# Performance work log

Measured on AMD Instinct MI355X. Metric: run time of the kernel, lower is better.

## Reference

```python
import jax, jax.numpy as jnp
import numpy as np


def make_dictionary(T, Drr, Dtheta):
    # rows i=0..T-1; (-Drr)**i == (-1)**i * Drr**i for integer i
    idx = jnp.arange(T, dtype=Drr.dtype)[:, None]                      # [T,1]
    sign = jnp.where(jnp.arange(T)[:, None] % 2 == 0, 1.0, -1.0).astype(Drr.dtype)
    ri = Drr[None, :] ** idx                                           # [T,N]
    c = jnp.cos(idx * Dtheta[None, :])
    s = jnp.sin(idx * Dtheta[None, :])
    dic = jnp.concatenate(
        [jnp.ones((T, 1), Drr.dtype), ri * c, sign * ri * c, ri * s, sign * ri * s],
        axis=1,
    )                                                                  # [T, 1+4N]
    G = jnp.linalg.norm(dic, axis=0)
    G = jnp.where(G == 0, jnp.sqrt(jnp.asarray(T, dic.dtype)), G)
    return dic / G


def softshrink(x, lam):
    return jnp.sign(x) * jnp.maximum(jnp.abs(x) - lam, 0.0)


def fista(D, Y, lambd=0.1, max_iter=100, tol=1e-4):
    # D: [T,K], Y: [B,T,F]
    K = D.shape[1]
    DtD = D.T @ D                                                      # [K,K]
    linv = 1.0 / jnp.linalg.norm(DtD)  # torch.norm(DtD, 2) == Frobenius norm
    DtY = jnp.einsum('tk,btf->bkf', D, Y) * linv                       # [B,K,F]
    A = jnp.eye(K, dtype=D.dtype) - DtD * linv
    lam = lambd * linv
    x0 = jnp.zeros_like(DtY)

    def cond(s):
        _, _, _, it, done = s
        return (it < max_iter) & jnp.logical_not(done)

    def body(s):
        x_old, y_old, t, it, done = s
        x_new = softshrink(jnp.einsum('kj,bjf->bkf', A, y_old) + DtY, lam)
        t_new = (1.0 + jnp.sqrt(1.0 + 4.0 * t * t)) / 2.0
        tt = (t - 1.0) / t_new
        y_new = (1.0 + tt) * x_new - tt * x_old
        conv = jnp.linalg.norm((x_new - x_old).ravel()) / K < tol
        return (x_new, y_new, jnp.where(conv, t, t_new), it + 1, conv)

    s0 = (x0, x0, jnp.asarray(1.0, D.dtype), jnp.asarray(0, jnp.int32),
          jnp.asarray(False))
    x, _, _, _, _ = jax.lax.while_loop(cond, body, s0)
    return x


def setup_inputs() -> dict:
    key = jax.random.key(0)
    k1, k2, k3 = jax.random.split(key, 3)
    return {
        'x': jax.random.normal(k1, (2, 36, 20480), jnp.float32),
        'Drr': jax.random.uniform(k2, (40,), dtype=jnp.float32),
        'Dtheta': jax.random.uniform(k3, (40,), dtype=jnp.float32),
        'T': 36,
    }


def reference(x, Drr, Dtheta, T):
    D = make_dictionary(T, Drr, Dtheta)
    return fista(D, x, lambd=0.1, max_iter=100)
```

## Files before the change

kernel.cpp:

```cpp
#include <hip/hip_runtime.h>
#include <math.h>

typedef _Float16 half8 __attribute__((ext_vector_type(8)));
typedef _Float16 half4 __attribute__((ext_vector_type(4)));
typedef __fp16   fp16x2 __attribute__((ext_vector_type(2)));
typedef float    f32x4 __attribute__((ext_vector_type(4)));

#define T_DIM 36
#define N_AT 40
#define K_REAL 161
#define MT 11
#define KSM 5
#define KS2 2
#define B_DIM 2
#define F_DIM 20480
#define CB 32
#define NTHREADS 256
#define SETUP_T 512
#define MAXIT 100
#define YK 200
#define YST 72

#define WS_AFRAG_OFF 64
#define AFRAG_BYTES (MT * KSM * 2 * 1024)
#define WS_DFRAG_OFF (WS_AFRAG_OFF + AFRAG_BYTES)
#define DFRAG_BYTES (MT * KS2 * 2 * 1024)
#define WS_A160_OFF (WS_DFRAG_OFF + DFRAG_BYTES)

#define MFMA16(a, b, c) __builtin_amdgcn_mfma_f32_16x16x32_f16((a), (b), (c), 0, 0, 0)

__global__ void setup_kernel(const float* __restrict__ Drr,
                             const float* __restrict__ Dtheta,
                             float* __restrict__ ws) {
    __shared__ float Dl[K_REAL][T_DIM];
    __shared__ float red[SETUP_T];
    __shared__ float s_linv;
    int tid = threadIdx.x;

    if (tid < K_REAL) {
        float col[T_DIM];
        if (tid == 0) {
            for (int i = 0; i < T_DIM; ++i) col[i] = 1.0f;
        } else {
            int q = (tid - 1) / N_AT, n = (tid - 1) % N_AT;
            float r = Drr[n], th = Dtheta[n];
            float ri = 1.0f;
            for (int i = 0; i < T_DIM; ++i) {
                float c = cosf((float)i * th), s = sinf((float)i * th);
                float sign = (i & 1) ? -1.0f : 1.0f;
                float v;
                if (q == 0)      v = ri * c;
                else if (q == 1) v = sign * ri * c;
                else if (q == 2) v = ri * s;
                else             v = sign * ri * s;
                col[i] = v;
                ri *= r;
            }
        }
        float ss = 0.0f;
        for (int i = 0; i < T_DIM; ++i) ss += col[i] * col[i];
        float G = sqrtf(ss);
        float Ginv = (G == 0.0f) ? (1.0f / sqrtf((float)T_DIM)) : (1.0f / G);
        for (int i = 0; i < T_DIM; ++i) Dl[tid][i] = col[i] * Ginv;
    }
    __syncthreads();

    float local = 0.0f;
    for (int p = tid; p < K_REAL * K_REAL; p += SETUP_T) {
        int a = p / K_REAL, b = p % K_REAL;
        float dot = 0.0f;
        for (int i = 0; i < T_DIM; ++i) dot += Dl[a][i] * Dl[b][i];
        local += dot * dot;
    }
    red[tid] = local;
    __syncthreads();
    if (tid == 0) {
        float tot = 0.0f;
        for (int i = 0; i < SETUP_T; ++i) tot += red[i];
        float linv = 1.0f / sqrtf(tot);
        s_linv = linv;
        ws[0] = linv;
        ws[1] = 0.1f * linv;
    }
    __syncthreads();
    float linv = s_linv;

    _Float16* wsA = (_Float16*)((char*)ws + WS_AFRAG_OFF);
    int lane = tid >> 3, e = tid & 7;
    int fm = lane & 15, fq = lane >> 4;
    for (int p = 0; p < MT * KSM; ++p) {
        int Mt = p / KSM, ks = p % KSM;
        int m = Mt * 16 + fm;
        int k = ks * 32 + fq * 8 + e;
        float v = 0.0f;
        if (m < K_REAL) {
            float dot = 0.0f;
            for (int t = 0; t < T_DIM; ++t) dot += Dl[m][t] * Dl[k][t];
            v = ((m == k) ? 1.0f : 0.0f) - linv * dot;
        }
        _Float16 h = (_Float16)v;
        _Float16 l = (_Float16)(v - (float)h);
        int base = (p * 2) * 512 + lane * 8 + e;
        wsA[base]       = h;
        wsA[base + 512] = l;
    }

    _Float16* wsD = (_Float16*)((char*)ws + WS_DFRAG_OFF);
    for (int p = 0; p < MT * KS2; ++p) {
        int Mt = p / KS2, ks2 = p % KS2;
        int kr = Mt * 16 + fm;
        int t  = ks2 * 32 + fq * 8 + e;
        float v = (kr < K_REAL && t < T_DIM) ? linv * Dl[kr][t] : 0.0f;
        _Float16 h = (_Float16)v;
        _Float16 l = (_Float16)(v - (float)h);
        int base = (p * 2) * 512 + lane * 8 + e;
        wsD[base]       = h;
        wsD[base + 512] = l;
    }

    float* wsC = (float*)((char*)ws + WS_A160_OFF);
    if (tid < MT * 16) {
        int m = tid;
        float v = 0.0f;
        if (m < K_REAL) {
            float dot = 0.0f;
            for (int t = 0; t < T_DIM; ++t) dot += Dl[m][t] * Dl[160][t];
            v = ((m == 160) ? 1.0f : 0.0f) - linv * dot;
        }
        wsC[m] = v;
    }
}

template <int G>
__device__ __forceinline__ void sweep_g(f32x4 (&acc)[3], const f32x4 (&dty)[3],
                                        const half8 (&Af)[3][KSM][2],
                                        const float (&a160)[3][4],
                                        const _Float16 (*Yh)[YK],
                                        const _Float16 (*Yl)[YK],
                                        int cl, int quad, int mlc) {
    #pragma unroll
    for (int ks = 0; ks < KSM; ++ks) {
        half8 yh = *(const half8*)&Yh[G * 16 + cl][ks * 32 + quad * 8];
        half8 yl = *(const half8*)&Yl[G * 16 + cl][ks * 32 + quad * 8];
        #pragma unroll
        for (int ml = 0; ml < 3; ++ml) {
            if (ml < mlc) {
                f32x4 c0 = (ks == 0) ? dty[ml] : acc[ml];
                c0 = MFMA16(Af[ml][ks][0], yh, c0);
                c0 = MFMA16(Af[ml][ks][0], yl, c0);
                acc[ml] = MFMA16(Af[ml][ks][1], yh, c0);
            }
        }
    }
    float y160 = (float)Yh[G * 16 + cl][160] + (float)Yl[G * 16 + cl][160];
    #pragma unroll
    for (int ml = 0; ml < 3; ++ml)
        if (ml < mlc)
            #pragma unroll
            for (int r = 0; r < 4; ++r)
                acc[ml][r] += a160[ml][r] * y160;
}

template <int G>
__device__ __forceinline__ void epi_g(const f32x4 (&acc)[3], float (&xold)[3][4],
                                      _Float16 (*Yh)[YK], _Float16 (*Yl)[YK],
                                      float lam, float tt,
                                      int cl, int quad, int mg, int mlc) {
    #pragma unroll
    for (int ml = 0; ml < 3; ++ml) {
        if (ml < mlc) {
            float yn[4];
            #pragma unroll
            for (int r = 0; r < 4; ++r) {
                float v  = acc[ml][r];
                float s  = fmaxf(fabsf(v) - lam, 0.0f);
                float xn = copysignf(s, v);
                yn[r] = xn + tt * (xn - xold[ml][r]);
                xold[ml][r] = xn;
            }
            fp16x2 h01 = __builtin_amdgcn_cvt_pkrtz(yn[0], yn[1]);
            fp16x2 h23 = __builtin_amdgcn_cvt_pkrtz(yn[2], yn[3]);
            float l0 = yn[0] - (float)h01[0];
            float l1 = yn[1] - (float)h01[1];
            float l2 = yn[2] - (float)h23[0];
            float l3 = yn[3] - (float)h23[1];
            fp16x2 l01 = __builtin_amdgcn_cvt_pkrtz(l0, l1);
            fp16x2 l23 = __builtin_amdgcn_cvt_pkrtz(l2, l3);
            half4 hv, lv;
            hv[0] = (_Float16)h01[0]; hv[1] = (_Float16)h01[1];
            hv[2] = (_Float16)h23[0]; hv[3] = (_Float16)h23[1];
            lv[0] = (_Float16)l01[0]; lv[1] = (_Float16)l01[1];
            lv[2] = (_Float16)l23[0]; lv[3] = (_Float16)l23[1];
            int k0 = (mg * 3 + ml) * 16 + quad * 4;
            *(half4*)&Yh[G * 16 + cl][k0] = hv;
            *(half4*)&Yl[G * 16 + cl][k0] = lv;
        }
    }
}

__global__ void __launch_bounds__(NTHREADS, 2)
fista_mfma(const float* __restrict__ Y, const float* __restrict__ ws,
           float* __restrict__ out) {
    __shared__ __align__(16) _Float16 Yh[CB][YK];
    __shared__ __align__(16) _Float16 Yl[CB][YK];

    const float lam = ((const float*)ws)[1];
    const half8* Afp = (const half8*)((const char*)ws + WS_AFRAG_OFF);
    const half8* Dfp = (const half8*)((const char*)ws + WS_DFRAG_OFF);
    const float* A160 = (const float*)((const char*)ws + WS_A160_OFF);

    const int tid  = threadIdx.x;
    const int lane = tid & 63;
    const int mg   = __builtin_amdgcn_readfirstlane(tid >> 6);
    const int mlc  = (mg == 3) ? 2 : 3;
    const int quad = lane >> 4;
    const int cl   = lane & 15;

    const int blk = blockIdx.x;
    const int b   = blk / (F_DIM / CB);
    const int f0  = (blk % (F_DIM / CB)) * CB;

    _Float16* sh = &Yh[0][0];
    _Float16* sl = &Yl[0][0];
    const float* Yb = Y + (size_t)b * T_DIM * F_DIM + f0;
    for (int idx = tid; idx < 64 * CB; idx += NTHREADS) {
        int t = idx / CB, c = idx % CB;
        float v = (t < T_DIM) ? Yb[(size_t)t * F_DIM + c] : 0.0f;
        _Float16 h = (_Float16)v;
        _Float16 l = (_Float16)(v - (float)h);
        sh[c * YST + t] = h;
        sl[c * YST + t] = l;
    }
    __syncthreads();

    f32x4 dty[2][3];
    #pragma unroll
    for (int g = 0; g < 2; ++g)
        #pragma unroll
        for (int ml = 0; ml < 3; ++ml) dty[g][ml] = f32x4{0.f, 0.f, 0.f, 0.f};
    #pragma unroll
    for (int ks2 = 0; ks2 < KS2; ++ks2) {
        #pragma unroll
        for (int g = 0; g < 2; ++g) {
            half8 yh = *(const half8*)&sh[(g * 16 + cl) * YST + ks2 * 32 + quad * 8];
            half8 yl = *(const half8*)&sl[(g * 16 + cl) * YST + ks2 * 32 + quad * 8];
            #pragma unroll
            for (int ml = 0; ml < 3; ++ml) {
                if (ml < mlc) {
                    int Mt = mg * 3 + ml;
                    half8 dh = Dfp[((Mt * KS2 + ks2) * 2 + 0) * 64 + lane];
                    half8 dl = Dfp[((Mt * KS2 + ks2) * 2 + 1) * 64 + lane];
                    dty[g][ml] = MFMA16(dh, yh, dty[g][ml]);
                    dty[g][ml] = MFMA16(dh, yl, dty[g][ml]);
                    dty[g][ml] = MFMA16(dl, yh, dty[g][ml]);
                }
            }
        }
    }
    __syncthreads();

    {
        int4* z1 = (int4*)&Yh[0][0];
        int4* z2 = (int4*)&Yl[0][0];
        for (int idx = tid; idx < (CB * YK * 2) / 16; idx += NTHREADS) {
            z1[idx] = int4{0, 0, 0, 0};
            z2[idx] = int4{0, 0, 0, 0};
        }
    }

    half8 Af[3][KSM][2];
    float a160[3][4];
    #pragma unroll
    for (int ml = 0; ml < 3; ++ml) {
        if (ml < mlc) {
            #pragma unroll
            for (int ks = 0; ks < KSM; ++ks)
                #pragma unroll
                for (int term = 0; term < 2; ++term)
                    Af[ml][ks][term] =
                        Afp[(((mg * 3 + ml) * KSM + ks) * 2 + term) * 64 + lane];
            #pragma unroll
            for (int r = 0; r < 4; ++r)
                a160[ml][r] = A160[(mg * 3 + ml) * 16 + quad * 4 + r];
        }
    }
    __syncthreads();

    float xoldA[3][4], xoldB[3][4];
    #pragma unroll
    for (int ml = 0; ml < 3; ++ml)
        #pragma unroll
        for (int r = 0; r < 4; ++r) { xoldA[ml][r] = 0.0f; xoldB[ml][r] = 0.0f; }

    f32x4 accA[3], accB[3];
    #pragma unroll
    for (int ml = 0; ml < 3; ++ml) { accA[ml] = dty[0][ml]; accB[ml] = dty[1][ml]; }

    float tm = 1.61803398875f;
    float tt_prev = 0.0f;

    epi_g<0>(accA, xoldA, Yh, Yl, lam, tt_prev, cl, quad, mg, mlc);
    __syncthreads();

    for (int s = 2; s <= MAXIT; ++s) {
        float tn = 0.5f * (1.0f + sqrtf(1.0f + 4.0f * tm * tm));
        float tt_cur = (tm - 1.0f) / tn;
        tm = tn;

        sweep_g<0>(accA, dty[0], Af, a160, Yh, Yl, cl, quad, mlc);
        epi_g<1>(accB, xoldB, Yh, Yl, lam, tt_prev, cl, quad, mg, mlc);
        __syncthreads();

        sweep_g<1>(accB, dty[1], Af, a160, Yh, Yl, cl, quad, mlc);
        epi_g<0>(accA, xoldA, Yh, Yl, lam, tt_cur, cl, quad, mg, mlc);
        __syncthreads();

        tt_prev = tt_cur;
    }
    epi_g<1>(accB, xoldB, Yh, Yl, lam, tt_prev, cl, quad, mg, mlc);

    #pragma unroll
    for (int g = 0; g < 2; ++g) {
        float* ob = out + (size_t)b * K_REAL * F_DIM + f0 + g * 16 + cl;
        #pragma unroll
        for (int ml = 0; ml < 3; ++ml)
            if (ml < mlc)
                #pragma unroll
                for (int r = 0; r < 4; ++r) {
                    int k = (mg * 3 + ml) * 16 + quad * 4 + r;
                    float xv = g ? xoldB[ml][r] : xoldA[ml][r];
                    if (k < K_REAL) ob[(size_t)k * F_DIM] = xv;
                }
    }
}

extern "C" void kernel_launch(void* const* d_in, const int* in_sizes, int n_in,
                              void* d_out, int out_size, void* d_ws, size_t ws_size,
                              hipStream_t stream) {
    const float* x      = (const float*)d_in[0];
    const float* Drr    = (const float*)d_in[1];
    const float* Dtheta = (const float*)d_in[2];
    float* out = (float*)d_out;
    float* ws  = (float*)d_ws;

    hipLaunchKernelGGL(setup_kernel, dim3(1), dim3(SETUP_T), 0, stream,
                       Drr, Dtheta, ws);
    hipLaunchKernelGGL(fista_mfma, dim3((B_DIM * F_DIM) / CB), dim3(NTHREADS),
                       0, stream, x, ws, out);
}
```

Measured before the change: 674.2 us.

## Switch FISTA iteration to 32x32 MFMA with double-buffered swizzled LDS

Replaces the 16x16x32 MFMA tiling (4 waves, two interleaved column groups, separate k=160 scalar fixup) with 32x32x16 MFMA tiles across 6 waves covering K padded to 192. The Y iterate is double-buffered in LDS with an XOR swizzle, so each iteration needs one barrier instead of two. The goal is fewer MFMA issues per FLOP, no scalar tail correction, fewer bank conflicts and less synchronisation. The cost is padding waste (192 vs 161 rows), more threads per block and higher register pressure from the 16-wide accumulators and 22 A fragments, plus a change in occupancy target.

```diff
diff --git a/kernel.cpp b/kernel.cpp
--- a/kernel.cpp
+++ b/kernel.cpp
@@ -4,30 +4,29 @@
 typedef _Float16 half8 __attribute__((ext_vector_type(8)));
 typedef _Float16 half4 __attribute__((ext_vector_type(4)));
 typedef __fp16   fp16x2 __attribute__((ext_vector_type(2)));
-typedef float    f32x4 __attribute__((ext_vector_type(4)));
+typedef float    f32x16 __attribute__((ext_vector_type(16)));
 
 #define T_DIM 36
 #define N_AT 40
 #define K_REAL 161
-#define MT 11
-#define KSM 5
-#define KS2 2
+#define MT2 6
+#define KS 11
+#define TKS 3
 #define B_DIM 2
 #define F_DIM 20480
 #define CB 32
-#define NTHREADS 256
+#define NTHREADS 384
 #define SETUP_T 512
 #define MAXIT 100
 #define YK 200
 #define YST 72
 
 #define WS_AFRAG_OFF 64
-#define AFRAG_BYTES (MT * KSM * 2 * 1024)
+#define AFRAG_BYTES (MT2 * KS * 2 * 1024)
 #define WS_DFRAG_OFF (WS_AFRAG_OFF + AFRAG_BYTES)
-#define DFRAG_BYTES (MT * KS2 * 2 * 1024)
-#define WS_A160_OFF (WS_DFRAG_OFF + DFRAG_BYTES)
-
-#define MFMA16(a, b, c) __builtin_amdgcn_mfma_f32_16x16x32_f16((a), (b), (c), 0, 0, 0)
+#define DFRAG_BYTES (MT2 * TKS * 2 * 1024)
+
+#define MFMA32(a, b, c) __builtin_amdgcn_mfma_f32_32x32x16_f16((a), (b), (c), 0, 0, 0)
 
 __global__ void setup_kernel(const float* __restrict__ Drr,
                              const float* __restrict__ Dtheta,
@@ -87,13 +86,13 @@
 
     _Float16* wsA = (_Float16*)((char*)ws + WS_AFRAG_OFF);
     int lane = tid >> 3, e = tid & 7;
-    int fm = lane & 15, fq = lane >> 4;
-    for (int p = 0; p < MT * KSM; ++p) {
-        int Mt = p / KSM, ks = p % KSM;
-        int m = Mt * 16 + fm;
-        int k = ks * 32 + fq * 8 + e;
+    int lm = lane & 31, lhi = lane >> 5;
+    for (int p = 0; p < MT2 * KS; ++p) {
+        int Mt = p / KS, ks = p % KS;
+        int m = Mt * 32 + lm;
+        int k = ks * 16 + lhi * 8 + e;
         float v = 0.0f;
-        if (m < K_REAL) {
+        if (m < K_REAL && k < K_REAL) {
             float dot = 0.0f;
             for (int t = 0; t < T_DIM; ++t) dot += Dl[m][t] * Dl[k][t];
             v = ((m == k) ? 1.0f : 0.0f) - linv * dot;
@@ -106,10 +105,10 @@
     }
 
     _Float16* wsD = (_Float16*)((char*)ws + WS_DFRAG_OFF);
-    for (int p = 0; p < MT * KS2; ++p) {
-        int Mt = p / KS2, ks2 = p % KS2;
-        int kr = Mt * 16 + fm;
-        int t  = ks2 * 32 + fq * 8 + e;
+    for (int p = 0; p < MT2 * TKS; ++p) {
+        int Mt = p / TKS, ks2 = p % TKS;
+        int kr = Mt * 32 + lm;
+        int t  = ks2 * 16 + lhi * 8 + e;
         float v = (kr < K_REAL && t < T_DIM) ? linv * Dl[kr][t] : 0.0f;
         _Float16 h = (_Float16)v;
         _Float16 l = (_Float16)(v - (float)h);
@@ -117,221 +116,143 @@
         wsD[base]       = h;
         wsD[base + 512] = l;
     }
-
-    float* wsC = (float*)((char*)ws + WS_A160_OFF);
-    if (tid < MT * 16) {
-        int m = tid;
-        float v = 0.0f;
-        if (m < K_REAL) {
-            float dot = 0.0f;
-            for (int t = 0; t < T_DIM; ++t) dot += Dl[m][t] * Dl[160][t];
-            v = ((m == 160) ? 1.0f : 0.0f) - linv * dot;
-        }
-        wsC[m] = v;
-    }
-}
-
-template <int G>
-__device__ __forceinline__ void sweep_g(f32x4 (&acc)[3], const f32x4 (&dty)[3],
-                                        const half8 (&Af)[3][KSM][2],
-                                        const float (&a160)[3][4],
-                                        const _Float16 (*Yh)[YK],
-                                        const _Float16 (*Yl)[YK],
-                                        int cl, int quad, int mlc) {
-    #pragma unroll
-    for (int ks = 0; ks < KSM; ++ks) {
-        half8 yh = *(const half8*)&Yh[G * 16 + cl][ks * 32 + quad * 8];
-        half8 yl = *(const half8*)&Yl[G * 16 + cl][ks * 32 + quad * 8];
-        #pragma unroll
-        for (int ml = 0; ml < 3; ++ml) {
-            if (ml < mlc) {
-                f32x4 c0 = (ks == 0) ? dty[ml] : acc[ml];
-                c0 = MFMA16(Af[ml][ks][0], yh, c0);
-                c0 = MFMA16(Af[ml][ks][0], yl, c0);
-                acc[ml] = MFMA16(Af[ml][ks][1], yh, c0);
-            }
-        }
-    }
-    float y160 = (float)Yh[G * 16 + cl][160] + (float)Yl[G * 16 + cl][160];
-    #pragma unroll
-    for (int ml = 0; ml < 3; ++ml)
-        if (ml < mlc)
-            #pragma unroll
-            for (int r = 0; r < 4; ++r)
-                acc[ml][r] += a160[ml][r] * y160;
-}
-
-template <int G>
-__device__ __forceinline__ void epi_g(const f32x4 (&acc)[3], float (&xold)[3][4],
-                                      _Float16 (*Yh)[YK], _Float16 (*Yl)[YK],
-                                      float lam, float tt,
-                                      int cl, int quad, int mg, int mlc) {
-    #pragma unroll
-    for (int ml = 0; ml < 3; ++ml) {
-        if (ml < mlc) {
-            float yn[4];
-            #pragma unroll
-            for (int r = 0; r < 4; ++r) {
-                float v  = acc[ml][r];
-                float s  = fmaxf(fabsf(v) - lam, 0.0f);
-                float xn = copysignf(s, v);
-                yn[r] = xn + tt * (xn - xold[ml][r]);
-                xold[ml][r] = xn;
-            }
-            fp16x2 h01 = __builtin_amdgcn_cvt_pkrtz(yn[0], yn[1]);
-            fp16x2 h23 = __builtin_amdgcn_cvt_pkrtz(yn[2], yn[3]);
-            float l0 = yn[0] - (float)h01[0];
-            float l1 = yn[1] - (float)h01[1];
-            float l2 = yn[2] - (float)h23[0];
-            float l3 = yn[3] - (float)h23[1];
-            fp16x2 l01 = __builtin_amdgcn_cvt_pkrtz(l0, l1);
-            fp16x2 l23 = __builtin_amdgcn_cvt_pkrtz(l2, l3);
-            half4 hv, lv;
-            hv[0] = (_Float16)h01[0]; hv[1] = (_Float16)h01[1];
-            hv[2] = (_Float16)h23[0]; hv[3] = (_Float16)h23[1];
-            lv[0] = (_Float16)l01[0]; lv[1] = (_Float16)l01[1];
-            lv[2] = (_Float16)l23[0]; lv[3] = (_Float16)l23[1];
-            int k0 = (mg * 3 + ml) * 16 + quad * 4;
-            *(half4*)&Yh[G * 16 + cl][k0] = hv;
-            *(half4*)&Yl[G * 16 + cl][k0] = lv;
-        }
-    }
-}
-
-__global__ void __launch_bounds__(NTHREADS, 2)
+}
+
+__device__ __forceinline__ void epi_write(const f32x16& acc, float (&xold)[16],
+                                          _Float16* rowH, _Float16* rowL,
+                                          float lam, float tt,
+                                          int wv, int sw, int hi) {
+    #pragma unroll
+    for (int g = 0; g < 4; ++g) {
+        float yn[4];
+        #pragma unroll
+        for (int i = 0; i < 4; ++i) {
+            int r = g * 4 + i;
+            float v  = acc[r];
+            float s  = fmaxf(fabsf(v) - lam, 0.0f);
+            float xn = copysignf(s, v);
+            yn[i] = xn + tt * (xn - xold[r]);
+            xold[r] = xn;
+        }
+        fp16x2 h01 = __builtin_amdgcn_cvt_pkrtz(yn[0], yn[1]);
+        fp16x2 h23 = __builtin_amdgcn_cvt_pkrtz(yn[2], yn[3]);
+        float l0 = yn[0] - (float)h01[0];
+        float l1 = yn[1] - (float)h01[1];
+        float l2 = yn[2] - (float)h23[0];
+        float l3 = yn[3] - (float)h23[1];
+        fp16x2 l01 = __builtin_amdgcn_cvt_pkrtz(l0, l1);
+        fp16x2 l23 = __builtin_amdgcn_cvt_pkrtz(l2, l3);
+        half4 hv, lv;
+        hv[0] = (_Float16)h01[0]; hv[1] = (_Float16)h01[1];
+        hv[2] = (_Float16)h23[0]; hv[3] = (_Float16)h23[1];
+        lv[0] = (_Float16)l01[0]; lv[1] = (_Float16)l01[1];
+        lv[2] = (_Float16)l23[0]; lv[3] = (_Float16)l23[1];
+        int boff = (((wv * 4 + g) ^ sw) << 4) + (hi << 3);
+        *(half4*)((char*)rowH + boff) = hv;
+        *(half4*)((char*)rowL + boff) = lv;
+    }
+}
+
+__global__ void __launch_bounds__(NTHREADS, 3)
 fista_mfma(const float* __restrict__ Y, const float* __restrict__ ws,
            float* __restrict__ out) {
-    __shared__ __align__(16) _Float16 Yh[CB][YK];
-    __shared__ __align__(16) _Float16 Yl[CB][YK];
+    __shared__ __align__(16) _Float16 Yb_lds[2][2][CB][YK];
 
     const float lam = ((const float*)ws)[1];
     const half8* Afp = (const half8*)((const char*)ws + WS_AFRAG_OFF);
     const half8* Dfp = (const half8*)((const char*)ws + WS_DFRAG_OFF);
-    const float* A160 = (const float*)((const char*)ws + WS_A160_OFF);
 
     const int tid  = threadIdx.x;
     const int lane = tid & 63;
-    const int mg   = __builtin_amdgcn_readfirstlane(tid >> 6);
-    const int mlc  = (mg == 3) ? 2 : 3;
-    const int quad = lane >> 4;
-    const int cl   = lane & 15;
+    const int wv   = __builtin_amdgcn_readfirstlane(tid >> 6);
+    const int c    = lane & 31;
+    const int hi   = lane >> 5;
+    const int sw   = (c >> 3) & 3;
 
     const int blk = blockIdx.x;
     const int b   = blk / (F_DIM / CB);
     const int f0  = (blk % (F_DIM / CB)) * CB;
 
-    _Float16* sh = &Yh[0][0];
-    _Float16* sl = &Yl[0][0];
+    _Float16* sh = &Yb_lds[0][0][0][0];
+    _Float16* sl = &Yb_lds[0][1][0][0];
     const float* Yb = Y + (size_t)b * T_DIM * F_DIM + f0;
-    for (int idx = tid; idx < 64 * CB; idx += NTHREADS) {
-        int t = idx / CB, c = idx % CB;
-        float v = (t < T_DIM) ? Yb[(size_t)t * F_DIM + c] : 0.0f;
+    for (int idx = tid; idx < 48 * CB; idx += NTHREADS) {
+        int t = idx >> 5, cc = idx & 31;
+        float v = (t < T_DIM) ? Yb[(size_t)t * F_DIM + cc] : 0.0f;
         _Float16 h = (_Float16)v;
         _Float16 l = (_Float16)(v - (float)h);
-        sh[c * YST + t] = h;
-        sl[c * YST + t] = l;
-    }
-    __syncthreads();
-
-    f32x4 dty[2][3];
-    #pragma unroll
-    for (int g = 0; g < 2; ++g)
-        #pragma unroll
-        for (int ml = 0; ml < 3; ++ml) dty[g][ml] = f32x4{0.f, 0.f, 0.f, 0.f};
-    #pragma unroll
-    for (int ks2 = 0; ks2 < KS2; ++ks2) {
-        #pragma unroll
-        for (int g = 0; g < 2; ++g) {
-            half8 yh = *(const half8*)&sh[(g * 16 + cl) * YST + ks2 * 32 + quad * 8];
-            half8 yl = *(const half8*)&sl[(g * 16 + cl) * YST + ks2 * 32 + quad * 8];
-            #pragma unroll
-            for (int ml = 0; ml < 3; ++ml) {
-                if (ml < mlc) {
-                    int Mt = mg * 3 + ml;
-                    half8 dh = Dfp[((Mt * KS2 + ks2) * 2 + 0) * 64 + lane];
-                    half8 dl = Dfp[((Mt * KS2 + ks2) * 2 + 1) * 64 + lane];
-                    dty[g][ml] = MFMA16(dh, yh, dty[g][ml]);
-                    dty[g][ml] = MFMA16(dh, yl, dty[g][ml]);
-                    dty[g][ml] = MFMA16(dl, yh, dty[g][ml]);
-                }
-            }
-        }
-    }
-    __syncthreads();
-
-    {
-        int4* z1 = (int4*)&Yh[0][0];
-        int4* z2 = (int4*)&Yl[0][0];
-        for (int idx = tid; idx < (CB * YK * 2) / 16; idx += NTHREADS) {
-            z1[idx] = int4{0, 0, 0, 0};
-            z2[idx] = int4{0, 0, 0, 0};
-        }
-    }
-
-    half8 Af[3][KSM][2];
-    float a160[3][4];
-    #pragma unroll
-    for (int ml = 0; ml < 3; ++ml) {
-        if (ml < mlc) {
-            #pragma unroll
-            for (int ks = 0; ks < KSM; ++ks)
-                #pragma unroll
-                for (int term = 0; term < 2; ++term)
-                    Af[ml][ks][term] =
-                        Afp[(((mg * 3 + ml) * KSM + ks) * 2 + term) * 64 + lane];
-            #pragma unroll
-            for (int r = 0; r < 4; ++r)
-                a160[ml][r] = A160[(mg * 3 + ml) * 16 + quad * 4 + r];
-        }
-    }
-    __syncthreads();
-
-    float xoldA[3][4], xoldB[3][4];
-    #pragma unroll
-    for (int ml = 0; ml < 3; ++ml)
-        #pragma unroll
-        for (int r = 0; r < 4; ++r) { xoldA[ml][r] = 0.0f; xoldB[ml][r] = 0.0f; }
-
-    f32x4 accA[3], accB[3];
-    #pragma unroll
-    for (int ml = 0; ml < 3; ++ml) { accA[ml] = dty[0][ml]; accB[ml] = dty[1][ml]; }
+        sh[cc * YST + t] = h;
+        sl[cc * YST + t] = l;
+    }
+    __syncthreads();
+
+    f32x16 dty;
+    #pragma unroll
+    for (int i = 0; i < 16; ++i) dty[i] = 0.0f;
+    #pragma unroll
+    for (int ks2 = 0; ks2 < TKS; ++ks2) {
+        half8 yh = *(const half8*)&sh[c * YST + ks2 * 16 + hi * 8];
+        half8 yl = *(const half8*)&sl[c * YST + ks2 * 16 + hi * 8];
+        half8 dh = Dfp[((wv * TKS + ks2) * 2 + 0) * 64 + lane];
+        half8 dl = Dfp[((wv * TKS + ks2) * 2 + 1) * 64 + lane];
+        dty = MFMA32(dh, yh, dty);
+        dty = MFMA32(dh, yl, dty);
+        dty = MFMA32(dl, yh, dty);
+    }
+    __syncthreads();
+
+    half8 Af[KS][2];
+    #pragma unroll
+    for (int ks = 0; ks < KS; ++ks)
+        #pragma unroll
+        for (int term = 0; term < 2; ++term)
+            Af[ks][term] = Afp[((wv * KS + ks) * 2 + term) * 64 + lane];
+
+    float xold[16];
+    #pragma unroll
+    for (int r = 0; r < 16; ++r) xold[r] = 0.0f;
+
+    f32x16 acc = dty;
 
     float tm = 1.61803398875f;
-    float tt_prev = 0.0f;
-
-    epi_g<0>(accA, xoldA, Yh, Yl, lam, tt_prev, cl, quad, mg, mlc);
+
+    epi_write(acc, xold, &Yb_lds[0][0][c][0], &Yb_lds[0][1][c][0],
+              lam, 0.0f, wv, sw, hi);
     __syncthreads();
 
     for (int s = 2; s <= MAXIT; ++s) {
         float tn = 0.5f * (1.0f + sqrtf(1.0f + 4.0f * tm * tm));
-        float tt_cur = (tm - 1.0f) / tn;
+        float tt = (tm - 1.0f) / tn;
         tm = tn;
 
-        sweep_g<0>(accA, dty[0], Af, a160, Yh, Yl, cl, quad, mlc);
-        epi_g<1>(accB, xoldB, Yh, Yl, lam, tt_prev, cl, quad, mg, mlc);
+        const int p = s & 1;
+        const _Float16* rH = &Yb_lds[p][0][c][0];
+        const _Float16* rL = &Yb_lds[p][1][c][0];
+
+        #pragma unroll
+        for (int ks = 0; ks < KS; ++ks) {
+            int boff = ((2 * ks + hi) ^ sw) << 4;
+            half8 yh = *(const half8*)((const char*)rH + boff);
+            half8 yl = *(const half8*)((const char*)rL + boff);
+            f32x16 c0 = (ks == 0) ? dty : acc;
+            c0  = MFMA32(Af[ks][0], yh, c0);
+            c0  = MFMA32(Af[ks][0], yl, c0);
+            acc = MFMA32(Af[ks][1], yh, c0);
+        }
+
+        epi_write(acc, xold, &Yb_lds[p ^ 1][0][c][0], &Yb_lds[p ^ 1][1][c][0],
+                  lam, tt, wv, sw, hi);
         __syncthreads();
-
-        sweep_g<1>(accB, dty[1], Af, a160, Yh, Yl, cl, quad, mlc);
-        epi_g<0>(accA, xoldA, Yh, Yl, lam, tt_cur, cl, quad, mg, mlc);
-        __syncthreads();
-
-        tt_prev = tt_cur;
-    }
-    epi_g<1>(accB, xoldB, Yh, Yl, lam, tt_prev, cl, quad, mg, mlc);
-
-    #pragma unroll
-    for (int g = 0; g < 2; ++g) {
-        float* ob = out + (size_t)b * K_REAL * F_DIM + f0 + g * 16 + cl;
-        #pragma unroll
-        for (int ml = 0; ml < 3; ++ml)
-            if (ml < mlc)
-                #pragma unroll
-                for (int r = 0; r < 4; ++r) {
-                    int k = (mg * 3 + ml) * 16 + quad * 4 + r;
-                    float xv = g ? xoldB[ml][r] : xoldA[ml][r];
-                    if (k < K_REAL) ob[(size_t)k * F_DIM] = xv;
-                }
-    }
+    }
+
+    float* ob = out + (size_t)b * K_REAL * F_DIM + f0 + c;
+    #pragma unroll
+    for (int g = 0; g < 4; ++g)
+        #pragma unroll
+        for (int i = 0; i < 4; ++i) {
+            int k = wv * 32 + i + 8 * g + 4 * hi;
+            if (k < K_REAL) ob[(size_t)k * F_DIM] = xold[g * 4 + i];
+        }
 }
 
 extern "C" void kernel_launch(void* const* d_in, const int* in_sizes, int n_in,
```

Measured after the change: 915.5 us. 35.8% more time.

## Spread M-tiles over six waves and XOR-swizzle the LDS Y layout

Applied to the files above, without the earlier changes.

The block grows from 4 to 6 waves, each now owning 2 of the 11 M-tiles instead of 3, with launch bounds raised to 3 blocks per CU. This cuts per-wave MFMA work and register use per iteration and adds latency hiding. The shared Y buffers now use a 256-half row stride with an XOR swizzle on 16-byte chunks, to avoid LDS bank conflicts in both the sweep reads and the epilogue writes. The hi/lo fp16 split now uses plain casts instead of packed round-toward-zero converts. The trade-offs are more barrier participants, an uneven last wave that owns only one tile, and slightly different rounding in the split.

```diff
diff --git a/kernel.cpp b/kernel.cpp
--- a/kernel.cpp
+++ b/kernel.cpp
@@ -3,7 +3,6 @@
 
 typedef _Float16 half8 __attribute__((ext_vector_type(8)));
 typedef _Float16 half4 __attribute__((ext_vector_type(4)));
-typedef __fp16   fp16x2 __attribute__((ext_vector_type(2)));
 typedef float    f32x4 __attribute__((ext_vector_type(4)));
 
 #define T_DIM 36
@@ -15,10 +14,10 @@
 #define B_DIM 2
 #define F_DIM 20480
 #define CB 32
-#define NTHREADS 256
+#define NTHREADS 384
 #define SETUP_T 512
 #define MAXIT 100
-#define YK 200
+#define YROW 256
 #define YST 72
 
 #define WS_AFRAG_OFF 64
@@ -132,18 +131,22 @@
 }
 
 template <int G>
-__device__ __forceinline__ void sweep_g(f32x4 (&acc)[3], const f32x4 (&dty)[3],
-                                        const half8 (&Af)[3][KSM][2],
-                                        const float (&a160)[3][4],
-                                        const _Float16 (*Yh)[YK],
-                                        const _Float16 (*Yl)[YK],
+__device__ __forceinline__ void sweep_g(f32x4 (&acc)[2], const f32x4 (&dty)[2],
+                                        const half8 (&Af)[2][KSM][2],
+                                        const float (&a160)[2][4],
+                                        const _Float16* __restrict__ Yhp,
+                                        const _Float16* __restrict__ Ylp,
                                         int cl, int quad, int mlc) {
+    const int r  = G * 16 + cl;
+    const int rb = r * YROW;
+    const int sw = r & 7;
     #pragma unroll
     for (int ks = 0; ks < KSM; ++ks) {
-        half8 yh = *(const half8*)&Yh[G * 16 + cl][ks * 32 + quad * 8];
-        half8 yl = *(const half8*)&Yl[G * 16 + cl][ks * 32 + quad * 8];
-        #pragma unroll
-        for (int ml = 0; ml < 3; ++ml) {
+        int off = rb + (((ks * 4 + quad) ^ sw) << 3);
+        half8 yh = *(const half8*)&Yhp[off];
+        half8 yl = *(const half8*)&Ylp[off];
+        #pragma unroll
+        for (int ml = 0; ml < 2; ++ml) {
             if (ml < mlc) {
                 f32x4 c0 = (ks == 0) ? dty[ml] : acc[ml];
                 c0 = MFMA16(Af[ml][ks][0], yh, c0);
@@ -152,57 +155,53 @@
             }
         }
     }
-    float y160 = (float)Yh[G * 16 + cl][160] + (float)Yl[G * 16 + cl][160];
-    #pragma unroll
-    for (int ml = 0; ml < 3; ++ml)
+    int off160 = rb + ((20 ^ sw) << 3);
+    float y160 = (float)Yhp[off160] + (float)Ylp[off160];
+    #pragma unroll
+    for (int ml = 0; ml < 2; ++ml)
         if (ml < mlc)
             #pragma unroll
-            for (int r = 0; r < 4; ++r)
-                acc[ml][r] += a160[ml][r] * y160;
+            for (int rr = 0; rr < 4; ++rr)
+                acc[ml][rr] += a160[ml][rr] * y160;
 }
 
 template <int G>
-__device__ __forceinline__ void epi_g(const f32x4 (&acc)[3], float (&xold)[3][4],
-                                      _Float16 (*Yh)[YK], _Float16 (*Yl)[YK],
+__device__ __forceinline__ void epi_g(const f32x4 (&acc)[2], float (&xold)[2][4],
+                                      _Float16* __restrict__ Yhp,
+                                      _Float16* __restrict__ Ylp,
                                       float lam, float tt,
-                                      int cl, int quad, int mg, int mlc) {
-    #pragma unroll
-    for (int ml = 0; ml < 3; ++ml) {
+                                      int cl, int quad, int wv, int mlc) {
+    const int r  = G * 16 + cl;
+    const int rb = r * YROW;
+    const int sw = r & 7;
+    #pragma unroll
+    for (int ml = 0; ml < 2; ++ml) {
         if (ml < mlc) {
-            float yn[4];
-            #pragma unroll
-            for (int r = 0; r < 4; ++r) {
-                float v  = acc[ml][r];
+            half4 hv, lv;
+            #pragma unroll
+            for (int rr = 0; rr < 4; ++rr) {
+                float v  = acc[ml][rr];
                 float s  = fmaxf(fabsf(v) - lam, 0.0f);
                 float xn = copysignf(s, v);
-                yn[r] = xn + tt * (xn - xold[ml][r]);
-                xold[ml][r] = xn;
+                float yn = xn + tt * (xn - xold[ml][rr]);
+                xold[ml][rr] = xn;
+                _Float16 h = (_Float16)yn;
+                hv[rr] = h;
+                lv[rr] = (_Float16)(yn - (float)h);
             }
-            fp16x2 h01 = __builtin_amdgcn_cvt_pkrtz(yn[0], yn[1]);
-            fp16x2 h23 = __builtin_amdgcn_cvt_pkrtz(yn[2], yn[3]);
-            float l0 = yn[0] - (float)h01[0];
-            float l1 = yn[1] - (float)h01[1];
-            float l2 = yn[2] - (float)h23[0];
-            float l3 = yn[3] - (float)h23[1];
-            fp16x2 l01 = __builtin_amdgcn_cvt_pkrtz(l0, l1);
-            fp16x2 l23 = __builtin_amdgcn_cvt_pkrtz(l2, l3);
-            half4 hv, lv;
-            hv[0] = (_Float16)h01[0]; hv[1] = (_Float16)h01[1];
-            hv[2] = (_Float16)h23[0]; hv[3] = (_Float16)h23[1];
-            lv[0] = (_Float16)l01[0]; lv[1] = (_Float16)l01[1];
-            lv[2] = (_Float16)l23[0]; lv[3] = (_Float16)l23[1];
-            int k0 = (mg * 3 + ml) * 16 + quad * 4;
-            *(half4*)&Yh[G * 16 + cl][k0] = hv;
-            *(half4*)&Yl[G * 16 + cl][k0] = lv;
-        }
-    }
-}
-
-__global__ void __launch_bounds__(NTHREADS, 2)
+            int bib = (wv * 2 + ml) * 32 + quad * 8;
+            int off = rb + ((((bib >> 4) ^ sw) << 3) | ((bib & 15) >> 1));
+            *(half4*)&Yhp[off] = hv;
+            *(half4*)&Ylp[off] = lv;
+        }
+    }
+}
+
+__global__ void __launch_bounds__(NTHREADS, 3)
 fista_mfma(const float* __restrict__ Y, const float* __restrict__ ws,
            float* __restrict__ out) {
-    __shared__ __align__(16) _Float16 Yh[CB][YK];
-    __shared__ __align__(16) _Float16 Yl[CB][YK];
+    __shared__ __align__(16) _Float16 YhL[CB * YROW];
+    __shared__ __align__(16) _Float16 YlL[CB * YROW];
 
     const float lam = ((const float*)ws)[1];
     const half8* Afp = (const half8*)((const char*)ws + WS_AFRAG_OFF);
@@ -211,8 +210,8 @@
 
     const int tid  = threadIdx.x;
     const int lane = tid & 63;
-    const int mg   = __builtin_amdgcn_readfirstlane(tid >> 6);
-    const int mlc  = (mg == 3) ? 2 : 3;
+    const int wv   = __builtin_amdgcn_readfirstlane(tid >> 6);
+    const int mlc  = (wv == 5) ? 1 : 2;
     const int quad = lane >> 4;
     const int cl   = lane & 15;
 
@@ -220,8 +219,8 @@
     const int b   = blk / (F_DIM / CB);
     const int f0  = (blk % (F_DIM / CB)) * CB;
 
-    _Float16* sh = &Yh[0][0];
-    _Float16* sl = &Yl[0][0];
+    _Float16* sh = &YhL[0];
+    _Float16* sl = &YlL[0];
     const float* Yb = Y + (size_t)b * T_DIM * F_DIM + f0;
     for (int idx = tid; idx < 64 * CB; idx += NTHREADS) {
         int t = idx / CB, c = idx % CB;
@@ -233,11 +232,11 @@
     }
     __syncthreads();
 
-    f32x4 dty[2][3];
+    f32x4 dty[2][2];
     #pragma unroll
     for (int g = 0; g < 2; ++g)
         #pragma unroll
-        for (int ml = 0; ml < 3; ++ml) dty[g][ml] = f32x4{0.f, 0.f, 0.f, 0.f};
+        for (int ml = 0; ml < 2; ++ml) dty[g][ml] = f32x4{0.f, 0.f, 0.f, 0.f};
     #pragma unroll
     for (int ks2 = 0; ks2 < KS2; ++ks2) {
         #pragma unroll
@@ -245,9 +244,9 @@
             half8 yh = *(const half8*)&sh[(g * 16 + cl) * YST + ks2 * 32 + quad * 8];
             half8 yl = *(const half8*)&sl[(g * 16 + cl) * YST + ks2 * 32 + quad * 8];
             #pragma unroll
-            for (int ml = 0; ml < 3; ++ml) {
+            for (int ml = 0; ml < 2; ++ml) {
                 if (ml < mlc) {
-                    int Mt = mg * 3 + ml;
+                    int Mt = wv * 2 + ml;
                     half8 dh = Dfp[((Mt * KS2 + ks2) * 2 + 0) * 64 + lane];
                     half8 dl = Dfp[((Mt * KS2 + ks2) * 2 + 1) * 64 + lane];
                     dty[g][ml] = MFMA16(dh, yh, dty[g][ml]);
@@ -260,46 +259,46 @@
     __syncthreads();
 
     {
-        int4* z1 = (int4*)&Yh[0][0];
-        int4* z2 = (int4*)&Yl[0][0];
-        for (int idx = tid; idx < (CB * YK * 2) / 16; idx += NTHREADS) {
+        int4* z1 = (int4*)&YhL[0];
+        int4* z2 = (int4*)&YlL[0];
+        for (int idx = tid; idx < (CB * YROW) / 8; idx += NTHREADS) {
             z1[idx] = int4{0, 0, 0, 0};
             z2[idx] = int4{0, 0, 0, 0};
         }
     }
 
-    half8 Af[3][KSM][2];
-    float a160[3][4];
-    #pragma unroll
-    for (int ml = 0; ml < 3; ++ml) {
+    half8 Af[2][KSM][2];
+    float a160[2][4];
+    #pragma unroll
+    for (int ml = 0; ml < 2; ++ml) {
         if (ml < mlc) {
             #pragma unroll
             for (int ks = 0; ks < KSM; ++ks)
                 #pragma unroll
                 for (int term = 0; term < 2; ++term)
                     Af[ml][ks][term] =
-                        Afp[(((mg * 3 + ml) * KSM + ks) * 2 + term) * 64 + lane];
-            #pragma unroll
-            for (int r = 0; r < 4; ++r)
-                a160[ml][r] = A160[(mg * 3 + ml) * 16 + quad * 4 + r];
-        }
-    }
-    __syncthreads();
-
-    float xoldA[3][4], xoldB[3][4];
-    #pragma unroll
-    for (int ml = 0; ml < 3; ++ml)
-        #pragma unroll
-        for (int r = 0; r < 4; ++r) { xoldA[ml][r] = 0.0f; xoldB[ml][r] = 0.0f; }
-
-    f32x4 accA[3], accB[3];
-    #pragma unroll
-    for (int ml = 0; ml < 3; ++ml) { accA[ml] = dty[0][ml]; accB[ml] = dty[1][ml]; }
+                        Afp[(((wv * 2 + ml) * KSM + ks) * 2 + term) * 64 + lane];
+            #pragma unroll
+            for (int rr = 0; rr < 4; ++rr)
+                a160[ml][rr] = A160[(wv * 2 + ml) * 16 + quad * 4 + rr];
+        }
+    }
+    __syncthreads();
+
+    float xoldA[2][4], xoldB[2][4];
+    #pragma unroll
+    for (int ml = 0; ml < 2; ++ml)
+        #pragma unroll
+        for (int rr = 0; rr < 4; ++rr) { xoldA[ml][rr] = 0.0f; xoldB[ml][rr] = 0.0f; }
+
+    f32x4 accA[2], accB[2];
+    #pragma unroll
+    for (int ml = 0; ml < 2; ++ml) { accA[ml] = dty[0][ml]; accB[ml] = dty[1][ml]; }
 
     float tm = 1.61803398875f;
     float tt_prev = 0.0f;
 
-    epi_g<0>(accA, xoldA, Yh, Yl, lam, tt_prev, cl, quad, mg, mlc);
+    epi_g<0>(accA, xoldA, YhL, YlL, lam, tt_prev, cl, quad, wv, mlc);
     __syncthreads();
 
     for (int s = 2; s <= MAXIT; ++s) {
@@ -307,28 +306,28 @@
         float tt_cur = (tm - 1.0f) / tn;
         tm = tn;
 
-        sweep_g<0>(accA, dty[0], Af, a160, Yh, Yl, cl, quad, mlc);
-        epi_g<1>(accB, xoldB, Yh, Yl, lam, tt_prev, cl, quad, mg, mlc);
+        sweep_g<0>(accA, dty[0], Af, a160, YhL, YlL, cl, quad, mlc);
+        epi_g<1>(accB, xoldB, YhL, YlL, lam, tt_prev, cl, quad, wv, mlc);
         __syncthreads();
 
-        sweep_g<1>(accB, dty[1], Af, a160, Yh, Yl, cl, quad, mlc);
-        epi_g<0>(accA, xoldA, Yh, Yl, lam, tt_cur, cl, quad, mg, mlc);
+        sweep_g<1>(accB, dty[1], Af, a160, YhL, YlL, cl, quad, mlc);
+        epi_g<0>(accA, xoldA, YhL, YlL, lam, tt_cur, cl, quad, wv, mlc);
         __syncthreads();
 
         tt_prev = tt_cur;
     }
-    epi_g<1>(accB, xoldB, Yh, Yl, lam, tt_prev, cl, quad, mg, mlc);
+    epi_g<1>(accB, xoldB, YhL, YlL, lam, tt_prev, cl, quad, wv, mlc);
 
     #pragma unroll
     for (int g = 0; g < 2; ++g) {
         float* ob = out + (size_t)b * K_REAL * F_DIM + f0 + g * 16 + cl;
         #pragma unroll
-        for (int ml = 0; ml < 3; ++ml)
+        for (int ml = 0; ml < 2; ++ml)
             if (ml < mlc)
                 #pragma unroll
-                for (int r = 0; r < 4; ++r) {
-                    int k = (mg * 3 + ml) * 16 + quad * 4 + r;
-                    float xv = g ? xoldB[ml][r] : xoldA[ml][r];
+                for (int rr = 0; rr < 4; ++rr) {
+                    int k = (wv * 2 + ml) * 16 + quad * 4 + rr;
+                    float xv = g ? xoldB[ml][rr] : xoldA[ml][rr];
                     if (k < K_REAL) ob[(size_t)k * F_DIM] = xv;
                 }
     }
```

Result: slower. 1.008 ms (+49.5%).

## Store FISTA y-state in MFMA fragment-native LDS layout with separate k=160 slot

Applied to the files above, without the earlier changes.

Replaces the row-major [CB][YK] fp16 hi/lo LDS buffers with per-group slabs laid out in MFMA B-fragment order, so each lane loads its half8 operand with a contiguous, conflict-free access indexed by lane. The padded k=160 row is moved to a small separate array written only by quad 0. The LDS zero-fill and one barrier are dropped, and the soft-threshold is rewritten as v - clamp(v,-lam,lam), with plain conversions replacing the packed round-toward-zero ones. This aims to cut LDS bank conflicts and epilogue ALU work. It relies on the tail rows never being read uninitialized and changes fp16 rounding mode.

```diff
diff --git a/kernel.cpp b/kernel.cpp
--- a/kernel.cpp
+++ b/kernel.cpp
@@ -3,7 +3,6 @@
 
 typedef _Float16 half8 __attribute__((ext_vector_type(8)));
 typedef _Float16 half4 __attribute__((ext_vector_type(4)));
-typedef __fp16   fp16x2 __attribute__((ext_vector_type(2)));
 typedef float    f32x4 __attribute__((ext_vector_type(4)));
 
 #define T_DIM 36
@@ -18,8 +17,8 @@
 #define NTHREADS 256
 #define SETUP_T 512
 #define MAXIT 100
-#define YK 200
 #define YST 72
+#define FSLAB (KSM * 512)
 
 #define WS_AFRAG_OFF 64
 #define AFRAG_BYTES (MT * KSM * 2 * 1024)
@@ -135,13 +134,15 @@
 __device__ __forceinline__ void sweep_g(f32x4 (&acc)[3], const f32x4 (&dty)[3],
                                         const half8 (&Af)[3][KSM][2],
                                         const float (&a160)[3][4],
-                                        const _Float16 (*Yh)[YK],
-                                        const _Float16 (*Yl)[YK],
-                                        int cl, int quad, int mlc) {
+                                        const _Float16 (*YF)[2][FSLAB],
+                                        const _Float16 (*Y160s)[16],
+                                        int lane, int cl, int mlc) {
+    const half8* fh = (const half8*)&YF[G][0][0];
+    const half8* fl = (const half8*)&YF[G][1][0];
     #pragma unroll
     for (int ks = 0; ks < KSM; ++ks) {
-        half8 yh = *(const half8*)&Yh[G * 16 + cl][ks * 32 + quad * 8];
-        half8 yl = *(const half8*)&Yl[G * 16 + cl][ks * 32 + quad * 8];
+        half8 yh = fh[ks * 64 + lane];
+        half8 yl = fl[ks * 64 + lane];
         #pragma unroll
         for (int ml = 0; ml < 3; ++ml) {
             if (ml < mlc) {
@@ -152,7 +153,7 @@
             }
         }
     }
-    float y160 = (float)Yh[G * 16 + cl][160] + (float)Yl[G * 16 + cl][160];
+    float y160 = (float)Y160s[2 * G + 0][cl] + (float)Y160s[2 * G + 1][cl];
     #pragma unroll
     for (int ml = 0; ml < 3; ++ml)
         if (ml < mlc)
@@ -163,37 +164,42 @@
 
 template <int G>
 __device__ __forceinline__ void epi_g(const f32x4 (&acc)[3], float (&xold)[3][4],
-                                      _Float16 (*Yh)[YK], _Float16 (*Yl)[YK],
+                                      _Float16 (*YF)[2][FSLAB],
+                                      _Float16 (*Y160s)[16],
                                       float lam, float tt,
                                       int cl, int quad, int mg, int mlc) {
+    char* ph = (char*)&YF[G][0][0];
+    char* pl = (char*)&YF[G][1][0];
     #pragma unroll
     for (int ml = 0; ml < 3; ++ml) {
         if (ml < mlc) {
-            float yn[4];
-            #pragma unroll
-            for (int r = 0; r < 4; ++r) {
-                float v  = acc[ml][r];
-                float s  = fmaxf(fabsf(v) - lam, 0.0f);
-                float xn = copysignf(s, v);
-                yn[r] = xn + tt * (xn - xold[ml][r]);
-                xold[ml][r] = xn;
+            const int t = mg * 3 + ml;
+            if (t < 10) {
+                half4 hv, lv;
+                #pragma unroll
+                for (int r = 0; r < 4; ++r) {
+                    float v  = acc[ml][r];
+                    float xn = v - fminf(fmaxf(v, -lam), lam);
+                    float yn = xn + tt * (xn - xold[ml][r]);
+                    xold[ml][r] = xn;
+                    _Float16 h = (_Float16)yn;
+                    hv[r] = h;
+                    lv[r] = (_Float16)(yn - (float)h);
+                }
+                int off = t * 512 + ((quad >> 1) << 8) + (cl << 4) + ((quad & 1) << 3);
+                *(half4*)(ph + off) = hv;
+                *(half4*)(pl + off) = lv;
+            } else {
+                if (quad == 0) {
+                    float v  = acc[ml][0];
+                    float xn = v - fminf(fmaxf(v, -lam), lam);
+                    float yn = xn + tt * (xn - xold[ml][0]);
+                    xold[ml][0] = xn;
+                    _Float16 h = (_Float16)yn;
+                    Y160s[2 * G + 0][cl] = h;
+                    Y160s[2 * G + 1][cl] = (_Float16)(yn - (float)h);
+                }
             }
-            fp16x2 h01 = __builtin_amdgcn_cvt_pkrtz(yn[0], yn[1]);
-            fp16x2 h23 = __builtin_amdgcn_cvt_pkrtz(yn[2], yn[3]);
-            float l0 = yn[0] - (float)h01[0];
-            float l1 = yn[1] - (float)h01[1];
-            float l2 = yn[2] - (float)h23[0];
-            float l3 = yn[3] - (float)h23[1];
-            fp16x2 l01 = __builtin_amdgcn_cvt_pkrtz(l0, l1);
-            fp16x2 l23 = __builtin_amdgcn_cvt_pkrtz(l2, l3);
-            half4 hv, lv;
-            hv[0] = (_Float16)h01[0]; hv[1] = (_Float16)h01[1];
-            hv[2] = (_Float16)h23[0]; hv[3] = (_Float16)h23[1];
-            lv[0] = (_Float16)l01[0]; lv[1] = (_Float16)l01[1];
-            lv[2] = (_Float16)l23[0]; lv[3] = (_Float16)l23[1];
-            int k0 = (mg * 3 + ml) * 16 + quad * 4;
-            *(half4*)&Yh[G * 16 + cl][k0] = hv;
-            *(half4*)&Yl[G * 16 + cl][k0] = lv;
         }
     }
 }
@@ -201,8 +207,8 @@
 __global__ void __launch_bounds__(NTHREADS, 2)
 fista_mfma(const float* __restrict__ Y, const float* __restrict__ ws,
            float* __restrict__ out) {
-    __shared__ __align__(16) _Float16 Yh[CB][YK];
-    __shared__ __align__(16) _Float16 Yl[CB][YK];
+    __shared__ __align__(16) _Float16 YF[2][2][FSLAB];
+    __shared__ __align__(16) _Float16 Y160s[4][16];
 
     const float lam = ((const float*)ws)[1];
     const half8* Afp = (const half8*)((const char*)ws + WS_AFRAG_OFF);
@@ -220,8 +226,8 @@
     const int b   = blk / (F_DIM / CB);
     const int f0  = (blk % (F_DIM / CB)) * CB;
 
-    _Float16* sh = &Yh[0][0];
-    _Float16* sl = &Yl[0][0];
+    _Float16* sh = &YF[0][0][0];
+    _Float16* sl = &YF[0][1][0];
     const float* Yb = Y + (size_t)b * T_DIM * F_DIM + f0;
     for (int idx = tid; idx < 64 * CB; idx += NTHREADS) {
         int t = idx / CB, c = idx % CB;
@@ -259,15 +265,6 @@
     }
     __syncthreads();
 
-    {
-        int4* z1 = (int4*)&Yh[0][0];
-        int4* z2 = (int4*)&Yl[0][0];
-        for (int idx = tid; idx < (CB * YK * 2) / 16; idx += NTHREADS) {
-            z1[idx] = int4{0, 0, 0, 0};
-            z2[idx] = int4{0, 0, 0, 0};
-        }
-    }
-
     half8 Af[3][KSM][2];
     float a160[3][4];
     #pragma unroll
@@ -284,7 +281,6 @@
                 a160[ml][r] = A160[(mg * 3 + ml) * 16 + quad * 4 + r];
         }
     }
-    __syncthreads();
 
     float xoldA[3][4], xoldB[3][4];
     #pragma unroll
@@ -299,7 +295,7 @@
     float tm = 1.61803398875f;
     float tt_prev = 0.0f;
 
-    epi_g<0>(accA, xoldA, Yh, Yl, lam, tt_prev, cl, quad, mg, mlc);
+    epi_g<0>(accA, xoldA, YF, Y160s, lam, tt_prev, cl, quad, mg, mlc);
     __syncthreads();
 
     for (int s = 2; s <= MAXIT; ++s) {
@@ -307,17 +303,17 @@
         float tt_cur = (tm - 1.0f) / tn;
         tm = tn;
 
-        sweep_g<0>(accA, dty[0], Af, a160, Yh, Yl, cl, quad, mlc);
-        epi_g<1>(accB, xoldB, Yh, Yl, lam, tt_prev, cl, quad, mg, mlc);
+        sweep_g<0>(accA, dty[0], Af, a160, YF, Y160s, lane, cl, mlc);
+        epi_g<1>(accB, xoldB, YF, Y160s, lam, tt_prev, cl, quad, mg, mlc);
         __syncthreads();
 
-        sweep_g<1>(accB, dty[1], Af, a160, Yh, Yl, cl, quad, mlc);
-        epi_g<0>(accA, xoldA, Yh, Yl, lam, tt_cur, cl, quad, mg, mlc);
+        sweep_g<1>(accB, dty[1], Af, a160, YF, Y160s, lane, cl, mlc);
+        epi_g<0>(accA, xoldA, YF, Y160s, lam, tt_cur, cl, quad, mg, mlc);
         __syncthreads();
 
         tt_prev = tt_cur;
     }
-    epi_g<1>(accB, xoldB, Yh, Yl, lam, tt_prev, cl, quad, mg, mlc);
+    epi_g<1>(accB, xoldB, YF, Y160s, lam, tt_prev, cl, quad, mg, mlc);
 
     #pragma unroll
     for (int g = 0; g < 2; ++g) {
```

Measured after the change: 707.1 us. +4.9%, slower.
